# Optimization experiments

Hardware: AMD Instinct MI355X
Metric: run time of the kernel (lower is better)

## Reference

```python
import jax, jax.numpy as jnp
import numpy as np

D_IN, D, H, NL, DFF = 128, 256, 4, 4, 1024
N, B, L = 32768, 64, 672


def setup_inputs() -> dict:
    key = jax.random.key(0)
    ks = jax.random.split(key, 12)
    s = 0.02
    return {
        "dom_embeddings": jax.random.normal(ks[0], (N, D_IN), jnp.float32),
        "dom_to_event_idx": jax.random.randint(ks[1], (N,), 0, B, jnp.int32),
        "batch_size": B,
        "seq_len": L,
        "proj_w": jax.random.normal(ks[2], (D_IN, D), jnp.float32) * s,
        "proj_b": jnp.zeros((D,), jnp.float32),
        "cls_token": jax.random.normal(ks[3], (D,), jnp.float32),
        "ln1_g": jnp.ones((NL, D), jnp.float32),
        "ln1_b": jnp.zeros((NL, D), jnp.float32),
        "qkv_w": jax.random.normal(ks[4], (NL, D, 3 * D), jnp.float32) * s,
        "qkv_b": jnp.zeros((NL, 3 * D), jnp.float32),
        "out_w": jax.random.normal(ks[5], (NL, D, D), jnp.float32) * s,
        "out_b": jnp.zeros((NL, D), jnp.float32),
        "ln2_g": jnp.ones((NL, D), jnp.float32),
        "ln2_b": jnp.zeros((NL, D), jnp.float32),
        "ff1_w": jax.random.normal(ks[6], (NL, D, DFF), jnp.float32) * s,
        "ff1_b": jnp.zeros((NL, DFF), jnp.float32),
        "ff2_w": jax.random.normal(ks[7], (NL, DFF, D), jnp.float32) * s,
        "ff2_b": jnp.zeros((NL, D), jnp.float32),
        "head1_w": jax.random.normal(ks[8], (D, D), jnp.float32) * s,
        "head1_b": jnp.zeros((D,), jnp.float32),
        "head2_w": jax.random.normal(ks[9], (D, 3), jnp.float32) * s,
        "head2_b": jnp.zeros((3,), jnp.float32),
    }


def _ln(x, g, b):
    m = jnp.mean(x, axis=-1, keepdims=True)
    v = jnp.var(x, axis=-1, keepdims=True)
    return (x - m) / jnp.sqrt(v + 1e-5) * g + b


def _forward(dom_embeddings, proj_w, proj_b, cls_token, ln1_g, ln1_b, qkv_w, qkv_b,
             out_w, out_b, ln2_g, ln2_b, ff1_w, ff1_b, ff2_w, ff2_b,
             head1_w, head1_b, head2_w, head2_b, idx, batch_size, seq_len):
    n = idx.shape[0]
    d = proj_w.shape[1]
    dh = d // H
    x = dom_embeddings @ proj_w + proj_b  # (N, d)

    # per-segment rank (replaces the python for-loop): stable argsort + cumsum of counts
    counts = jnp.zeros((batch_size,), jnp.int32).at[idx].add(1)
    starts = jnp.cumsum(counts) - counts
    order = jnp.argsort(idx)  # jax sort is stable -> preserves in-event order
    rank_sorted = jnp.arange(n, dtype=jnp.int32) - starts[idx[order]]
    positions = jnp.zeros((n,), jnp.int32).at[order].set(rank_sorted)

    # scatter into padded batch; slot 0 is cls (note: cls KEY stays masked, as in torch code)
    bt = jnp.zeros((batch_size, seq_len, d), x.dtype).at[:, 0, :].set(cls_token)
    bt = bt.at[idx, positions + 1].set(x)
    pad = jnp.ones((batch_size, seq_len), bool).at[idx, positions + 1].set(False)
    bias = jnp.where(pad, -jnp.inf, 0.0).astype(x.dtype)[:, None, None, :]  # (B,1,1,L)

    h = bt
    for i in range(NL):  # norm_first pre-LN encoder layers
        y = _ln(h, ln1_g[i], ln1_b[i])
        qkv = y @ qkv_w[i] + qkv_b[i]
        q, k, v = jnp.split(qkv, 3, axis=-1)
        q = q.reshape(batch_size, seq_len, H, dh)
        k = k.reshape(batch_size, seq_len, H, dh)
        v = v.reshape(batch_size, seq_len, H, dh)
        scores = jnp.einsum('bqhd,bkhd->bhqk', q, k) * (1.0 / np.sqrt(dh))
        attn = jax.nn.softmax(scores + bias, axis=-1)
        o = jnp.einsum('bhqk,bkhd->bqhd', attn, v).reshape(batch_size, seq_len, d)
        h = h + o @ out_w[i] + out_b[i]
        z = _ln(h, ln2_g[i], ln2_b[i])
        h = h + jax.nn.relu(z @ ff1_w[i] + ff1_b[i]) @ ff2_w[i] + ff2_b[i]

    cls = h[:, 0, :]
    p = jax.nn.relu(cls @ head1_w + head1_b) @ head2_w + head2_b
    return p / jnp.sqrt(jnp.sum(p * p, axis=1, keepdims=True))


def reference(dom_embeddings, dom_to_event_idx, batch_size, seq_len, proj_w, proj_b,
              cls_token, ln1_g, ln1_b, qkv_w, qkv_b, out_w, out_b, ln2_g, ln2_b,
              ff1_w, ff1_b, ff2_w, ff2_b, head1_w, head1_b, head2_w, head2_b):
    return _forward(dom_embeddings, proj_w, proj_b, cls_token, ln1_g, ln1_b, qkv_w,
                    qkv_b, out_w, out_b, ln2_g, ln2_b, ff1_w, ff1_b, ff2_w, ff2_b,
                    head1_w, head1_b, head2_w, head2_b,
                    dom_to_event_idx, batch_size, seq_len)
```

## Files before the change

kernel.cpp:

```cpp
#include <hip/hip_runtime.h>
#include <cstdint>
#include <cstddef>

#define NDOM   32768
#define DIN    128
#define DMODEL 256
#define NHEAD  4
#define NLAYER 4
#define DFFN   1024
#define BATCH  64
#define SEQ    672
#define DHEAD  64
#define MROWS  (BATCH*SEQ)

typedef unsigned short u16;
typedef __attribute__((ext_vector_type(8))) short bf8;
typedef __attribute__((ext_vector_type(4))) float f4;

__device__ inline u16 f2b(float x) {
    union { float f; unsigned u; } c; c.f = x;
    unsigned r = c.u + 0x7fffu + ((c.u >> 16) & 1u);
    return (u16)(r >> 16);
}

__device__ inline void gload16(const void* g, const void* l) {
    __builtin_amdgcn_global_load_lds(
        (const __attribute__((address_space(1))) void*)g,
        (__attribute__((address_space(3))) void*)l, 16, 0, 0);
}


__global__ void k_zero_counts(int* __restrict__ counts) {
    if (threadIdx.x < BATCH) counts[threadIdx.x] = 0;
}

__global__ void k_pos(const int* __restrict__ idx, int* __restrict__ counts,
                      int* __restrict__ pos) {
    int i = blockIdx.x * blockDim.x + threadIdx.x;
    if (i < NDOM) pos[i] = atomicAdd(&counts[idx[i]], 1);
}

__global__ void k_init_h(float* __restrict__ h, const float* __restrict__ cls) {
    const float4* cls4 = (const float4*)cls;
    float4* h4 = (float4*)h;
    const int total4 = MROWS * DMODEL / 4;
    for (int f = blockIdx.x * blockDim.x + threadIdx.x; f < total4;
         f += gridDim.x * blockDim.x) {
        int d4 = f & 63;
        int t  = (f >> 6) % SEQ;
        h4[f] = (t == 0) ? cls4[d4] : make_float4(0.f, 0.f, 0.f, 0.f);
    }
}

__global__ void k_b16(const float* __restrict__ x, u16* __restrict__ y, int n4) {
    int i = blockIdx.x * 256 + threadIdx.x;
    if (i < n4) {
        float4 v = ((const float4*)x)[i];
        ushort4 o;
        o.x = f2b(v.x); o.y = f2b(v.y); o.z = f2b(v.z); o.w = f2b(v.w);
        ((ushort4*)y)[i] = o;
    }
}

__global__ __launch_bounds__(256) void k_wt_all(
    const float* __restrict__ projw, const float* __restrict__ qkvw,
    const float* __restrict__ outw,  const float* __restrict__ ff1w,
    const float* __restrict__ ff2w,
    u16* __restrict__ wpj, u16* __restrict__ wq, u16* __restrict__ wo,
    u16* __restrict__ w1,  u16* __restrict__ w2)
{
    __shared__ float t[64][65];
    const int tile = blockIdx.x;
    const float* W; u16* D; int K, N, local;
    if (tile < 8)        { W = projw; D = wpj; K = 128;  N = 256;  local = tile; }
    else if (tile < 200) { int l = (tile-8)/48;   local = (tile-8)%48;
                           W = qkvw + (size_t)l*196608; D = wq + (size_t)l*196608; K = 256;  N = 768; }
    else if (tile < 264) { int l = (tile-200)/16; local = (tile-200)%16;
                           W = outw + (size_t)l*65536;  D = wo + (size_t)l*65536;  K = 256;  N = 256; }
    else if (tile < 520) { int l = (tile-264)/64; local = (tile-264)%64;
                           W = ff1w + (size_t)l*262144; D = w1 + (size_t)l*262144; K = 256;  N = 1024; }
    else                 { int l = (tile-520)/64; local = (tile-520)%64;
                           W = ff2w + (size_t)l*262144; D = w2 + (size_t)l*262144; K = 1024; N = 256; }
    const int ntn = N >> 6;
    const int tk = local / ntn, tn = local % ntn;
    const int r = threadIdx.x >> 6, c = threadIdx.x & 63;
    #pragma unroll 4
    for (int rr = r; rr < 64; rr += 4)
        t[rr][c] = W[(size_t)(tk*64 + rr) * N + tn*64 + c];
    __syncthreads();
    #pragma unroll 4
    for (int rr = r; rr < 64; rr += 4)
        D[(size_t)(tn*64 + rr) * K + tk*64 + c] = f2b(t[c][rr]);
}

__global__ __launch_bounds__(256) void k_scatter(
    const float* __restrict__ xp, const int* __restrict__ idx,
    const int* __restrict__ pos, float* __restrict__ h)
{
    const int i = blockIdx.x * 4 + (threadIdx.x >> 6);
    const int lane = threadIdx.x & 63;
    const int p = pos[i] + 1;
    if (p >= SEQ) return;
    const size_t row = (size_t)idx[i] * SEQ + p;
    ((float4*)(h + row * DMODEL))[lane] = ((const float4*)(xp + (size_t)i * DMODEL))[lane];
}


__global__ __launch_bounds__(256) void k_ln_bf(
    const float* __restrict__ x, const float* __restrict__ g,
    const float* __restrict__ bt, u16* __restrict__ y)
{
    const int row  = blockIdx.x * 4 + (threadIdx.x >> 6);
    const int lane = threadIdx.x & 63;
    float4 v = ((const float4*)(x + (size_t)row * DMODEL))[lane];
    float s = v.x + v.y + v.z + v.w;
    #pragma unroll
    for (int off = 32; off >= 1; off >>= 1) s += __shfl_xor(s, off);
    const float m = s * (1.f / DMODEL);
    const float d0 = v.x - m, d1 = v.y - m, d2 = v.z - m, d3 = v.w - m;
    float q = d0*d0 + d1*d1 + d2*d2 + d3*d3;
    #pragma unroll
    for (int off = 32; off >= 1; off >>= 1) q += __shfl_xor(q, off);
    const float rstd = rsqrtf(q * (1.f / DMODEL) + 1e-5f);
    const float4 gv = ((const float4*)g)[lane];
    const float4 bv = ((const float4*)bt)[lane];
    ushort4 o;
    o.x = f2b(d0 * rstd * gv.x + bv.x);
    o.y = f2b(d1 * rstd * gv.y + bv.y);
    o.z = f2b(d2 * rstd * gv.z + bv.z);
    o.w = f2b(d3 * rstd * gv.w + bv.w);
    ((ushort4*)(y + (size_t)row * DMODEL))[lane] = o;
}


template<int RELU, int RESID, int OBF, int OF32>
__global__ __launch_bounds__(256) void k_gemm_bf(
    const u16* __restrict__ A, const u16* __restrict__ Bt,
    const float* __restrict__ bias, float* __restrict__ Cf,
    u16* __restrict__ Cb, int K, int N)
{
    __shared__ u16 As[8192];
    __shared__ u16 Bs[8192];
    const int tid = threadIdx.x;
    const int w = tid >> 6, lane = tid & 63;
    const int lr = lane & 15, lg = lane >> 4;
    const int m0 = blockIdx.y * 128, n0 = blockIdx.x * 128;
    const int wm = (w >> 1) * 64, wn = (w & 1) * 64;

    const f4 zf = {0.f, 0.f, 0.f, 0.f};
    f4 acc[4][4];
    #pragma unroll
    for (int i = 0; i < 4; ++i)
        #pragma unroll
        for (int j = 0; j < 4; ++j) acc[i][j] = zf;

    const int srow8 = lane >> 3;
    const int sq = lane & 7;

    for (int k0 = 0; k0 < K; k0 += 64) {
        #pragma unroll
        for (int c = 0; c < 4; ++c) {
            const int chunk = w * 4 + c;
            const int row = chunk * 8 + srow8;
            const int ks = k0 + ((sq ^ (row & 7)) << 3);
            gload16(A  + (size_t)(m0 + row) * K + ks, (const char*)As + chunk * 1024);
            gload16(Bt + (size_t)(n0 + row) * K + ks, (const char*)Bs + chunk * 1024);
        }
        __syncthreads();
        #pragma unroll
        for (int kk = 0; kk < 2; ++kk) {
            bf8 af[4], bg[4];
            #pragma unroll
            for (int f = 0; f < 4; ++f) {
                const int ra = wm + f * 16 + lr;
                af[f] = *(const bf8*)((const char*)As + ra * 128 +
                        ((((kk << 2) | lg) ^ (ra & 7)) << 4));
                const int rb = wn + f * 16 + lr;
                bg[f] = *(const bf8*)((const char*)Bs + rb * 128 +
                        ((((kk << 2) | lg) ^ (rb & 7)) << 4));
            }
            #pragma unroll
            for (int fm = 0; fm < 4; ++fm)
                #pragma unroll
                for (int fn = 0; fn < 4; ++fn)
                    acc[fm][fn] = __builtin_amdgcn_mfma_f32_16x16x32_bf16(
                        af[fm], bg[fn], acc[fm][fn], 0, 0, 0);
        }
        __syncthreads();
    }

    float bv[4];
    #pragma unroll
    for (int fn = 0; fn < 4; ++fn) bv[fn] = bias[n0 + wn + fn * 16 + lr];
    #pragma unroll
    for (int fm = 0; fm < 4; ++fm)
        #pragma unroll
        for (int j = 0; j < 4; ++j) {
            const int row = m0 + wm + fm * 16 + lg * 4 + j;
            #pragma unroll
            for (int fn = 0; fn < 4; ++fn) {
                float v = acc[fm][fn][j] + bv[fn];
                if (RELU) v = fmaxf(v, 0.f);
                const size_t off = (size_t)row * N + n0 + wn + fn * 16 + lr;
                if (RESID) Cf[off] += v;
                if (OF32)  Cf[off] = v;
                if (OBF)   Cb[off] = f2b(v);
            }
        }
}


template<int LNF>
__global__ __launch_bounds__(512) void k_gemm_ln(
    const u16* __restrict__ A, const u16* __restrict__ Bt,
    const float* __restrict__ bias, float* __restrict__ h,
    u16* __restrict__ ybf, const float* __restrict__ lng,
    const float* __restrict__ lnb, int K)
{
    __shared__ u16 As[8192];
    __shared__ u16 Bs[16384];
    __shared__ float red[8][136];
    const int tid = threadIdx.x;
    const int w = tid >> 6, lane = tid & 63;
    const int lr = lane & 15, lg = lane >> 4;
    const int m0 = blockIdx.x * 128;
    const int wm = (w >> 2) * 64, wn = (w & 3) * 64;

    const f4 zf = {0.f, 0.f, 0.f, 0.f};
    f4 acc[4][4];
    #pragma unroll
    for (int i = 0; i < 4; ++i)
        #pragma unroll
        for (int j = 0; j < 4; ++j) acc[i][j] = zf;

    const int srow8 = lane >> 3;
    const int sq = lane & 7;

    for (int k0 = 0; k0 < K; k0 += 64) {
        #pragma unroll
        for (int c = 0; c < 2; ++c) {
            const int chunk = w * 2 + c;
            const int row = chunk * 8 + srow8;
            const int ks = k0 + ((sq ^ (row & 7)) << 3);
            gload16(A + (size_t)(m0 + row) * K + ks, (const char*)As + chunk * 1024);
        }
        #pragma unroll
        for (int c = 0; c < 4; ++c) {
            const int chunk = w * 4 + c;
            const int row = chunk * 8 + srow8;
            const int ks = k0 + ((sq ^ (row & 7)) << 3);
            gload16(Bt + (size_t)row * K + ks, (const char*)Bs + chunk * 1024);
        }
        __syncthreads();
        #pragma unroll
        for (int kk = 0; kk < 2; ++kk) {
            bf8 af[4], bg[4];
            #pragma unroll
            for (int f = 0; f < 4; ++f) {
                const int ra = wm + f * 16 + lr;
                af[f] = *(const bf8*)((const char*)As + ra * 128 +
                        ((((kk << 2) | lg) ^ (ra & 7)) << 4));
                const int rb = wn + f * 16 + lr;
                bg[f] = *(const bf8*)((const char*)Bs + rb * 128 +
                        ((((kk << 2) | lg) ^ (rb & 7)) << 4));
            }
            #pragma unroll
            for (int fm = 0; fm < 4; ++fm)
                #pragma unroll
                for (int fn = 0; fn < 4; ++fn)
                    acc[fm][fn] = __builtin_amdgcn_mfma_f32_16x16x32_bf16(
                        af[fm], bg[fn], acc[fm][fn], 0, 0, 0);
        }
        __syncthreads();
    }

    float bv[4];
    #pragma unroll
    for (int fn = 0; fn < 4; ++fn) bv[fn] = bias[wn + fn * 16 + lr];
    float sr[4][4], s2r[4][4];
    #pragma unroll
    for (int fm = 0; fm < 4; ++fm)
        #pragma unroll
        for (int j = 0; j < 4; ++j) {
            const int row = m0 + wm + fm * 16 + lg * 4 + j;
            float s = 0.f, s2 = 0.f;
            #pragma unroll
            for (int fn = 0; fn < 4; ++fn) {
                float v = acc[fm][fn][j] + bv[fn];
                v += h[(size_t)row * DMODEL + wn + fn * 16 + lr];
                acc[fm][fn][j] = v;
                s += v; s2 += v * v;
            }
            if (LNF) {
                #pragma unroll
                for (int off = 1; off <= 8; off <<= 1) {
                    s  += __shfl_xor(s, off);
                    s2 += __shfl_xor(s2, off);
                }
            }
            sr[fm][j] = s; s2r[fm][j] = s2;
        }

    if (LNF) {
        if (lr == 0) {
            #pragma unroll
            for (int fm = 0; fm < 4; ++fm)
                #pragma unroll
                for (int j = 0; j < 4; ++j) {
                    const int rL = wm + fm * 16 + lg * 4 + j;
                    red[(w & 3) * 2 + 0][rL] = sr[fm][j];
                    red[(w & 3) * 2 + 1][rL] = s2r[fm][j];
                }
        }
        __syncthreads();
        float gl[4], bl[4];
        #pragma unroll
        for (int fn = 0; fn < 4; ++fn) {
            gl[fn] = lng[wn + fn * 16 + lr];
            bl[fn] = lnb[wn + fn * 16 + lr];
        }
        #pragma unroll
        for (int fm = 0; fm < 4; ++fm)
            #pragma unroll
            for (int j = 0; j < 4; ++j) {
                const int rL = wm + fm * 16 + lg * 4 + j;
                const int row = m0 + rL;
                const float S  = red[0][rL] + red[2][rL] + red[4][rL] + red[6][rL];
                const float S2 = red[1][rL] + red[3][rL] + red[5][rL] + red[7][rL];
                const float mean = S * (1.f / DMODEL);
                const float var  = S2 * (1.f / DMODEL) - mean * mean;
                const float rstd = rsqrtf(var + 1e-5f);
                #pragma unroll
                for (int fn = 0; fn < 4; ++fn) {
                    const float v = acc[fm][fn][j];
                    const size_t off = (size_t)row * DMODEL + wn + fn * 16 + lr;
                    h[off] = v;
                    ybf[off] = f2b((v - mean) * rstd * gl[fn] + bl[fn]);
                }
            }
    } else {
        #pragma unroll
        for (int fm = 0; fm < 4; ++fm)
            #pragma unroll
            for (int j = 0; j < 4; ++j) {
                const int row = m0 + wm + fm * 16 + lg * 4 + j;
                #pragma unroll
                for (int fn = 0; fn < 4; ++fn)
                    h[(size_t)row * DMODEL + wn + fn * 16 + lr] = acc[fm][fn][j];
            }
    }
}


__global__ __launch_bounds__(512) void k_attn_mfma(
    const u16* __restrict__ qkv, const int* __restrict__ counts,
    u16* __restrict__ out)
{
    __shared__ u16 Ks[4096];
    __shared__ u16 Vt[4096];
    __shared__ u16 Ps[8][1024];
    const int tid = threadIdx.x;
    const int w = tid >> 6, lane = tid & 63;
    const int lr = lane & 15, lg = lane >> 4;
    const int L = blockIdx.x;
    const int b = (L & 7) * 8 + (L >> 3) / 24;
    const int r = (L >> 3) % 24;
    const int qt = r >> 2, hh = r & 3;
    const int q0 = qt * 128;
    const int kmax = min(counts[b], SEQ - 1);
    if (q0 > kmax) return;
    const int ntiles = (kmax + 64) >> 6;
    const size_t bb = (size_t)b * SEQ;

    const int qrow = q0 + w * 16 + lr;
    const size_t qoff = (bb + (size_t)min(qrow, SEQ - 1)) * 768 + hh * 64 + (lg << 3);
    const bf8 qf0 = *(const bf8*)(qkv + qoff);
    const bf8 qf1 = *(const bf8*)(qkv + qoff + 32);

    const f4 zf = {0.f, 0.f, 0.f, 0.f};
    f4 o_[4];
    #pragma unroll
    for (int fn = 0; fn < 4; ++fn) o_[fn] = zf;
    float mrow = -INFINITY, ssum = 0.f;

    for (int kt = 0; kt < ntiles; ++kt) {
        const int k0 = kt * 64;
        {
            const int row = w * 8 + (lane >> 3);
            const int q = lane & 7;
            const int krow = min(k0 + row, SEQ - 1);
            gload16(qkv + (bb + krow) * 768 + 256 + hh * 64 + ((q ^ (row & 7)) << 3),
                    (const char*)Ks + w * 1024);
        }
        {
            const int kk2 = (tid & 31) * 2;
            const int dh0 = (tid >> 5) * 4;
            const int r0 = min(k0 + kk2, SEQ - 1), r1 = min(k0 + kk2 + 1, SEQ - 1);
            const ushort4 v0 = *(const ushort4*)(qkv + (bb + r0) * 768 + 512 + hh * 64 + dh0);
            const ushort4 v1 = *(const ushort4*)(qkv + (bb + r1) * 768 + 512 + hh * 64 + dh0);
            const u16* pv0 = (const u16*)&v0;
            const u16* pv1 = (const u16*)&v1;
            #pragma unroll
            for (int e = 0; e < 4; ++e) {
                const int d = dh0 + e;
                const unsigned pk = (unsigned)pv0[e] | ((unsigned)pv1[e] << 16);
                *(unsigned*)((char*)Vt + d * 128 +
                    ((((kk2 >> 3) ^ (d & 7)) << 4)) + ((kk2 & 7) << 1)) = pk;
            }
        }
        __syncthreads();

        f4 sf[4];
        #pragma unroll
        for (int fk = 0; fk < 4; ++fk) sf[fk] = zf;
        #pragma unroll
        for (int kk = 0; kk < 2; ++kk) {
            const bf8 qf = kk ? qf1 : qf0;
            #pragma unroll
            for (int fk = 0; fk < 4; ++fk) {
                const int rk = fk * 16 + lr;
                const bf8 kf = *(const bf8*)((const char*)Ks + rk * 128 +
                        ((((kk << 2) | lg) ^ (rk & 7)) << 4));
                sf[fk] = __builtin_amdgcn_mfma_f32_16x16x32_bf16(kf, qf, sf[fk], 0, 0, 0);
            }
        }

        float sv[4][4];
        float pmax = -INFINITY;
        if (k0 >= 1 && k0 + 63 <= kmax) {
            #pragma unroll
            for (int fk = 0; fk < 4; ++fk)
                #pragma unroll
                for (int j = 0; j < 4; ++j) {
                    const float x = sf[fk][j] * 0.125f;
                    sv[fk][j] = x;
                    pmax = fmaxf(pmax, x);
                }
        } else {
            #pragma unroll
            for (int fk = 0; fk < 4; ++fk)
                #pragma unroll
                for (int j = 0; j < 4; ++j) {
                    const int key = k0 + fk * 16 + lg * 4 + j;
                    const float x = (key >= 1 && key <= kmax) ? sf[fk][j] * 0.125f : -INFINITY;
                    sv[fk][j] = x;
                    pmax = fmaxf(pmax, x);
                }
        }
        pmax = fmaxf(pmax, __shfl_xor(pmax, 16));
        pmax = fmaxf(pmax, __shfl_xor(pmax, 32));
        const float mnew = fmaxf(mrow, pmax);
        const float fac = __expf(mrow - mnew);
        mrow = mnew;
        float tsum = 0.f;
        #pragma unroll
        for (int fk = 0; fk < 4; ++fk) {
            const float p0 = __expf(sv[fk][0] - mnew);
            const float p1 = __expf(sv[fk][1] - mnew);
            const float p2 = __expf(sv[fk][2] - mnew);
            const float p3 = __expf(sv[fk][3] - mnew);
            tsum += p0 + p1 + p2 + p3;
            ushort4 pk;
            pk.x = f2b(p0); pk.y = f2b(p1); pk.z = f2b(p2); pk.w = f2b(p3);
            *(ushort4*)((char*)Ps[w] + lr * 128 +
                (((((fk << 1) | (lg >> 1)) ^ (lr & 7)) << 4)) + ((lg & 1) << 3)) = pk;
        }
        tsum += __shfl_xor(tsum, 16);
        tsum += __shfl_xor(tsum, 32);
        ssum = ssum * fac + tsum;

        #pragma unroll
        for (int j = 0; j < 4; ++j) {
            const float fj = __shfl(fac, lg * 4 + j);
            #pragma unroll
            for (int fn = 0; fn < 4; ++fn) o_[fn][j] *= fj;
        }
        __syncthreads();

        #pragma unroll
        for (int kk = 0; kk < 2; ++kk) {
            const bf8 pa = *(const bf8*)((const char*)Ps[w] + lr * 128 +
                    ((((kk << 2) | lg) ^ (lr & 7)) << 4));
            #pragma unroll
            for (int fn = 0; fn < 4; ++fn) {
                const int rv = fn * 16 + lr;
                const bf8 vf = *(const bf8*)((const char*)Vt + rv * 128 +
                        ((((kk << 2) | lg) ^ (rv & 7)) << 4));
                o_[fn] = __builtin_amdgcn_mfma_f32_16x16x32_bf16(pa, vf, o_[fn], 0, 0, 0);
            }
        }
        __syncthreads();
    }

    const float inv = 1.f / ssum;
    #pragma unroll
    for (int j = 0; j < 4; ++j) {
        const float ij = __shfl(inv, lg * 4 + j);
        const int qr = q0 + w * 16 + lg * 4 + j;
        if (qr < SEQ) {
            #pragma unroll
            for (int fn = 0; fn < 4; ++fn)
                out[(bb + qr) * DMODEL + hh * 64 + fn * 16 + lr] = f2b(o_[fn][j] * ij);
        }
    }
}


__global__ __launch_bounds__(256) void k_head(
    const float* __restrict__ h, const float* __restrict__ w1,
    const float* __restrict__ b1, const float* __restrict__ w2,
    const float* __restrict__ b2, float* __restrict__ out)
{
    __shared__ float cbuf[DMODEL];
    __shared__ float p1[DMODEL];
    __shared__ float p2[3];
    const int b = blockIdx.x, tid = threadIdx.x;
    cbuf[tid] = h[(size_t)b * SEQ * DMODEL + tid];
    __syncthreads();
    float acc = b1[tid];
    #pragma unroll 8
    for (int k = 0; k < DMODEL; ++k) acc = fmaf(cbuf[k], w1[k * DMODEL + tid], acc);
    p1[tid] = fmaxf(acc, 0.f);
    __syncthreads();
    if (tid < 3) {
        float a = b2[tid];
        for (int k = 0; k < DMODEL; ++k) a = fmaf(p1[k], w2[k * 3 + tid], a);
        p2[tid] = a;
    }
    __syncthreads();
    if (tid < 3) {
        float n2 = p2[0]*p2[0] + p2[1]*p2[1] + p2[2]*p2[2];
        out[b * 3 + tid] = p2[tid] * rsqrtf(n2);
    }
}


extern "C" void kernel_launch(void* const* d_in, const int* in_sizes, int n_in,
                              void* d_out, int out_size, void* d_ws, size_t ws_size,
                              hipStream_t stream) {
    const float* emb   = (const float*)d_in[0];
    const int*   idx   = (const int*)d_in[1];
    const float* projw = (const float*)d_in[4];
    const float* projb = (const float*)d_in[5];
    const float* cls   = (const float*)d_in[6];
    const float* ln1g  = (const float*)d_in[7];
    const float* ln1b  = (const float*)d_in[8];
    const float* qkvw  = (const float*)d_in[9];
    const float* qkvb  = (const float*)d_in[10];
    const float* outw  = (const float*)d_in[11];
    const float* outb  = (const float*)d_in[12];
    const float* ln2g  = (const float*)d_in[13];
    const float* ln2b  = (const float*)d_in[14];
    const float* ff1w  = (const float*)d_in[15];
    const float* ff1b  = (const float*)d_in[16];
    const float* ff2w  = (const float*)d_in[17];
    const float* ff2b  = (const float*)d_in[18];
    const float* h1w   = (const float*)d_in[19];
    const float* h1b   = (const float*)d_in[20];
    const float* h2w   = (const float*)d_in[21];
    const float* h2b   = (const float*)d_in[22];
    float* out = (float*)d_out;

    char* ws = (char*)d_ws;
    int*   counts = (int*)ws;
    int*   pos    = (int*)(ws + 4096);
    float* h      = (float*)(ws + 135168);
    u16*   ybf    = (u16*)(ws + 44175360);
    u16*   qkvb16 = (u16*)(ws + 66195456);
    u16*   ffb    = (u16*)(ws + 132354048);
    u16*   wq     = (u16*)(ws + 220434432);
    u16*   wo     = (u16*)(ws + 222007296);
    u16*   w1     = (u16*)(ws + 222531584);
    u16*   w2     = (u16*)(ws + 224628736);
    u16*   wpj    = (u16*)(ws + 226725888);
    u16*   embbf  = qkvb16;
    float* xp     = (float*)ffb;

    k_zero_counts<<<1, 64, 0, stream>>>(counts);
    k_pos<<<NDOM / 256, 256, 0, stream>>>(idx, counts, pos);
    k_b16<<<(NDOM * DIN / 4) / 256, 256, 0, stream>>>(emb, embbf, NDOM * DIN / 4);
    k_wt_all<<<776, 256, 0, stream>>>(projw, qkvw, outw, ff1w, ff2w,
                                      wpj, wq, wo, w1, w2);
    k_init_h<<<2688, 256, 0, stream>>>(h, cls);
    k_gemm_bf<0,0,0,1><<<dim3(2, 256), 256, 0, stream>>>(
        embbf, wpj, projb, xp, nullptr, DIN, DMODEL);
    k_scatter<<<NDOM / 4, 256, 0, stream>>>(xp, idx, pos, h);
    k_ln_bf<<<MROWS / 4, 256, 0, stream>>>(h, ln1g, ln1b, ybf);

    for (int l = 0; l < NLAYER; ++l) {
        k_gemm_bf<0,0,1,0><<<dim3(6, 336), 256, 0, stream>>>(
            ybf, wq + (size_t)l * 196608, qkvb + l * 768, nullptr, qkvb16, 256, 768);
        k_attn_mfma<<<1536, 512, 0, stream>>>(qkvb16, counts, ybf);
        k_gemm_ln<1><<<336, 512, 0, stream>>>(
            ybf, wo + (size_t)l * 65536, outb + l * DMODEL, h, ybf,
            ln2g + l * DMODEL, ln2b + l * DMODEL, 256);
        k_gemm_bf<1,0,1,0><<<dim3(8, 336), 256, 0, stream>>>(
            ybf, w1 + (size_t)l * 262144, ff1b + l * DFFN, nullptr, ffb, 256, 1024);
        if (l < NLAYER - 1)
            k_gemm_ln<1><<<336, 512, 0, stream>>>(
                ffb, w2 + (size_t)l * 262144, ff2b + l * DMODEL, h, ybf,
                ln1g + (l + 1) * DMODEL, ln1b + (l + 1) * DMODEL, 1024);
        else
            k_gemm_ln<0><<<336, 512, 0, stream>>>(
                ffb, w2 + (size_t)l * 262144, ff2b + l * DMODEL, h, nullptr,
                nullptr, nullptr, 1024);
    }

    k_head<<<BATCH, 256, 0, stream>>>(h, h1w, h1b, h2w, h2b, out);
}
```

Before: 1.184 ms.

## Pack event rows contiguously to skip padded rows; lazy softmax rescaling

```diff
diff --git a/kernel.cpp b/kernel.cpp
--- a/kernel.cpp
+++ b/kernel.cpp
@@ -11,7 +11,8 @@
 #define BATCH  64
 #define SEQ    672
 #define DHEAD  64
-#define MROWS  (BATCH*SEQ)
+#define MC     33024
+#define MTILES 258
 
 typedef unsigned short u16;
 typedef __attribute__((ext_vector_type(8))) short bf8;
@@ -40,16 +41,31 @@
     if (i < NDOM) pos[i] = atomicAdd(&counts[idx[i]], 1);
 }
 
-__global__ void k_init_h(float* __restrict__ h, const float* __restrict__ cls) {
-    const float4* cls4 = (const float4*)cls;
-    float4* h4 = (float4*)h;
-    const int total4 = MROWS * DMODEL / 4;
-    for (int f = blockIdx.x * blockDim.x + threadIdx.x; f < total4;
-         f += gridDim.x * blockDim.x) {
-        int d4 = f & 63;
-        int t  = (f >> 6) % SEQ;
-        h4[f] = (t == 0) ? cls4[d4] : make_float4(0.f, 0.f, 0.f, 0.f);
-    }
+__global__ void k_base(const int* __restrict__ counts, int* __restrict__ base) {
+    const int lane = threadIdx.x;
+    const int c = counts[lane];
+    int s = c;
+    #pragma unroll
+    for (int off = 1; off < 64; off <<= 1) {
+        int t = __shfl_up(s, off);
+        if (lane >= off) s += t;
+    }
+    base[lane] = lane + (s - c);
+    if (lane == 63) base[64] = 64 + s;
+}
+
+__global__ void k_rmap(const int* __restrict__ idx, const int* __restrict__ pos,
+                       const int* __restrict__ base, int* __restrict__ rmap) {
+    int i = blockIdx.x * 256 + threadIdx.x;
+    if (i < NDOM) {
+        int p = pos[i] + 1;
+        rmap[i] = (p < SEQ) ? base[idx[i]] + p : (MC - 1);
+    }
+}
+
+__global__ void k_init_cls(const int* __restrict__ base, const float* __restrict__ cls,
+                           float* __restrict__ h) {
+    h[(size_t)base[blockIdx.x] * DMODEL + threadIdx.x] = cls[threadIdx.x];
 }
 
 __global__ void k_b16(const float* __restrict__ x, u16* __restrict__ y, int n4) {
@@ -93,18 +109,6 @@
         D[(size_t)(tn*64 + rr) * K + tk*64 + c] = f2b(t[c][rr]);
 }
 
-__global__ __launch_bounds__(256) void k_scatter(
-    const float* __restrict__ xp, const int* __restrict__ idx,
-    const int* __restrict__ pos, float* __restrict__ h)
-{
-    const int i = blockIdx.x * 4 + (threadIdx.x >> 6);
-    const int lane = threadIdx.x & 63;
-    const int p = pos[i] + 1;
-    if (p >= SEQ) return;
-    const size_t row = (size_t)idx[i] * SEQ + p;
-    ((float4*)(h + row * DMODEL))[lane] = ((const float4*)(xp + (size_t)i * DMODEL))[lane];
-}
-
 
 __global__ __launch_bounds__(256) void k_ln_bf(
     const float* __restrict__ x, const float* __restrict__ g,
@@ -133,11 +137,11 @@
 }
 
 
-template<int RELU, int RESID, int OBF, int OF32>
+template<int RELU, int OBF, int OF32, int SCAT>
 __global__ __launch_bounds__(256) void k_gemm_bf(
     const u16* __restrict__ A, const u16* __restrict__ Bt,
     const float* __restrict__ bias, float* __restrict__ Cf,
-    u16* __restrict__ Cb, int K, int N)
+    u16* __restrict__ Cb, const int* __restrict__ rmap, int K, int N)
 {
     __shared__ u16 As[8192];
     __shared__ u16 Bs[8192];
@@ -197,12 +201,12 @@
         #pragma unroll
         for (int j = 0; j < 4; ++j) {
             const int row = m0 + wm + fm * 16 + lg * 4 + j;
+            const int orow = SCAT ? rmap[row] : row;
             #pragma unroll
             for (int fn = 0; fn < 4; ++fn) {
                 float v = acc[fm][fn][j] + bv[fn];
                 if (RELU) v = fmaxf(v, 0.f);
-                const size_t off = (size_t)row * N + n0 + wn + fn * 16 + lr;
-                if (RESID) Cf[off] += v;
+                const size_t off = (size_t)orow * N + n0 + wn + fn * 16 + lr;
                 if (OF32)  Cf[off] = v;
                 if (OBF)   Cb[off] = f2b(v);
             }
@@ -354,7 +358,7 @@
 
 __global__ __launch_bounds__(512) void k_attn_mfma(
     const u16* __restrict__ qkv, const int* __restrict__ counts,
-    u16* __restrict__ out)
+    const int* __restrict__ base, u16* __restrict__ out)
 {
     __shared__ u16 Ks[4096];
     __shared__ u16 Vt[4096];
@@ -370,10 +374,10 @@
     const int kmax = min(counts[b], SEQ - 1);
     if (q0 > kmax) return;
     const int ntiles = (kmax + 64) >> 6;
-    const size_t bb = (size_t)b * SEQ;
+    const size_t bb = (size_t)base[b];
 
     const int qrow = q0 + w * 16 + lr;
-    const size_t qoff = (bb + (size_t)min(qrow, SEQ - 1)) * 768 + hh * 64 + (lg << 3);
+    const size_t qoff = (bb + qrow) * 768 + hh * 64 + (lg << 3);
     const bf8 qf0 = *(const bf8*)(qkv + qoff);
     const bf8 qf1 = *(const bf8*)(qkv + qoff + 32);
 
@@ -388,16 +392,14 @@
         {
             const int row = w * 8 + (lane >> 3);
             const int q = lane & 7;
-            const int krow = min(k0 + row, SEQ - 1);
-            gload16(qkv + (bb + krow) * 768 + 256 + hh * 64 + ((q ^ (row & 7)) << 3),
+            gload16(qkv + (bb + k0 + row) * 768 + 256 + hh * 64 + ((q ^ (row & 7)) << 3),
                     (const char*)Ks + w * 1024);
         }
         {
             const int kk2 = (tid & 31) * 2;
             const int dh0 = (tid >> 5) * 4;
-            const int r0 = min(k0 + kk2, SEQ - 1), r1 = min(k0 + kk2 + 1, SEQ - 1);
-            const ushort4 v0 = *(const ushort4*)(qkv + (bb + r0) * 768 + 512 + hh * 64 + dh0);
-            const ushort4 v1 = *(const ushort4*)(qkv + (bb + r1) * 768 + 512 + hh * 64 + dh0);
+            const ushort4 v0 = *(const ushort4*)(qkv + (bb + k0 + kk2) * 768 + 512 + hh * 64 + dh0);
+            const ushort4 v1 = *(const ushort4*)(qkv + (bb + k0 + kk2 + 1) * 768 + 512 + hh * 64 + dh0);
             const u16* pv0 = (const u16*)&v0;
             const u16* pv1 = (const u16*)&v1;
             #pragma unroll
@@ -449,16 +451,27 @@
         }
         pmax = fmaxf(pmax, __shfl_xor(pmax, 16));
         pmax = fmaxf(pmax, __shfl_xor(pmax, 32));
-        const float mnew = fmaxf(mrow, pmax);
-        const float fac = __expf(mrow - mnew);
-        mrow = mnew;
+
+        if (!__all(pmax <= mrow + 8.f)) {
+            const float mnew = fmaxf(mrow, pmax);
+            const float fac = __expf(mrow - mnew);
+            mrow = mnew;
+            ssum *= fac;
+            #pragma unroll
+            for (int j = 0; j < 4; ++j) {
+                const float fj = __shfl(fac, lg * 4 + j);
+                #pragma unroll
+                for (int fn = 0; fn < 4; ++fn) o_[fn][j] *= fj;
+            }
+        }
+
         float tsum = 0.f;
         #pragma unroll
         for (int fk = 0; fk < 4; ++fk) {
-            const float p0 = __expf(sv[fk][0] - mnew);
-            const float p1 = __expf(sv[fk][1] - mnew);
-            const float p2 = __expf(sv[fk][2] - mnew);
-            const float p3 = __expf(sv[fk][3] - mnew);
+            const float p0 = __expf(sv[fk][0] - mrow);
+            const float p1 = __expf(sv[fk][1] - mrow);
+            const float p2 = __expf(sv[fk][2] - mrow);
+            const float p3 = __expf(sv[fk][3] - mrow);
             tsum += p0 + p1 + p2 + p3;
             ushort4 pk;
             pk.x = f2b(p0); pk.y = f2b(p1); pk.z = f2b(p2); pk.w = f2b(p3);
@@ -467,14 +480,7 @@
         }
         tsum += __shfl_xor(tsum, 16);
         tsum += __shfl_xor(tsum, 32);
-        ssum = ssum * fac + tsum;
-
-        #pragma unroll
-        for (int j = 0; j < 4; ++j) {
-            const float fj = __shfl(fac, lg * 4 + j);
-            #pragma unroll
-            for (int fn = 0; fn < 4; ++fn) o_[fn][j] *= fj;
-        }
+        ssum += tsum;
         __syncthreads();
 
         #pragma unroll
@@ -497,7 +503,7 @@
     for (int j = 0; j < 4; ++j) {
         const float ij = __shfl(inv, lg * 4 + j);
         const int qr = q0 + w * 16 + lg * 4 + j;
-        if (qr < SEQ) {
+        if (qr <= kmax) {
             #pragma unroll
             for (int fn = 0; fn < 4; ++fn)
                 out[(bb + qr) * DMODEL + hh * 64 + fn * 16 + lr] = f2b(o_[fn][j] * ij);
@@ -507,15 +513,16 @@
 
 
 __global__ __launch_bounds__(256) void k_head(
-    const float* __restrict__ h, const float* __restrict__ w1,
-    const float* __restrict__ b1, const float* __restrict__ w2,
-    const float* __restrict__ b2, float* __restrict__ out)
+    const float* __restrict__ h, const int* __restrict__ base,
+    const float* __restrict__ w1, const float* __restrict__ b1,
+    const float* __restrict__ w2, const float* __restrict__ b2,
+    float* __restrict__ out)
 {
     __shared__ float cbuf[DMODEL];
     __shared__ float p1[DMODEL];
     __shared__ float p2[3];
     const int b = blockIdx.x, tid = threadIdx.x;
-    cbuf[tid] = h[(size_t)b * SEQ * DMODEL + tid];
+    cbuf[tid] = h[(size_t)base[b] * DMODEL + tid];
     __syncthreads();
     float acc = b1[tid];
     #pragma unroll 8
@@ -563,48 +570,50 @@
 
     char* ws = (char*)d_ws;
     int*   counts = (int*)ws;
-    int*   pos    = (int*)(ws + 4096);
-    float* h      = (float*)(ws + 135168);
-    u16*   ybf    = (u16*)(ws + 44175360);
-    u16*   qkvb16 = (u16*)(ws + 66195456);
-    u16*   ffb    = (u16*)(ws + 132354048);
-    u16*   wq     = (u16*)(ws + 220434432);
-    u16*   wo     = (u16*)(ws + 222007296);
-    u16*   w1     = (u16*)(ws + 222531584);
-    u16*   w2     = (u16*)(ws + 224628736);
-    u16*   wpj    = (u16*)(ws + 226725888);
-    u16*   embbf  = qkvb16;
-    float* xp     = (float*)ffb;
+    int*   base   = (int*)(ws + 256);
+    int*   pos    = (int*)(ws + 1024);
+    int*   rmap   = (int*)(ws + 132096);
+    float* h      = (float*)(ws + 263168);
+    u16*   ybf    = (u16*)(ws + 34079744);
+    u16*   qkvc   = (u16*)(ws + 50988032);
+    u16*   ffb    = (u16*)(ws + 101712896);
+    u16*   wq     = (u16*)(ws + 169346048);
+    u16*   wo     = (u16*)(ws + 170918912);
+    u16*   w1     = (u16*)(ws + 171443200);
+    u16*   w2     = (u16*)(ws + 173540352);
+    u16*   wpj    = (u16*)(ws + 175637504);
+    u16*   embbf  = qkvc;
 
     k_zero_counts<<<1, 64, 0, stream>>>(counts);
     k_pos<<<NDOM / 256, 256, 0, stream>>>(idx, counts, pos);
+    k_base<<<1, 64, 0, stream>>>(counts, base);
+    k_rmap<<<NDOM / 256, 256, 0, stream>>>(idx, pos, base, rmap);
     k_b16<<<(NDOM * DIN / 4) / 256, 256, 0, stream>>>(emb, embbf, NDOM * DIN / 4);
     k_wt_all<<<776, 256, 0, stream>>>(projw, qkvw, outw, ff1w, ff2w,
                                       wpj, wq, wo, w1, w2);
-    k_init_h<<<2688, 256, 0, stream>>>(h, cls);
-    k_gemm_bf<0,0,0,1><<<dim3(2, 256), 256, 0, stream>>>(
-        embbf, wpj, projb, xp, nullptr, DIN, DMODEL);
-    k_scatter<<<NDOM / 4, 256, 0, stream>>>(xp, idx, pos, h);
-    k_ln_bf<<<MROWS / 4, 256, 0, stream>>>(h, ln1g, ln1b, ybf);
+    k_init_cls<<<BATCH, 256, 0, stream>>>(base, cls, h);
+    k_gemm_bf<0,0,1,1><<<dim3(2, 256), 256, 0, stream>>>(
+        embbf, wpj, projb, h, nullptr, rmap, DIN, DMODEL);
+    k_ln_bf<<<MC / 4, 256, 0, stream>>>(h, ln1g, ln1b, ybf);
 
     for (int l = 0; l < NLAYER; ++l) {
-        k_gemm_bf<0,0,1,0><<<dim3(6, 336), 256, 0, stream>>>(
-            ybf, wq + (size_t)l * 196608, qkvb + l * 768, nullptr, qkvb16, 256, 768);
-        k_attn_mfma<<<1536, 512, 0, stream>>>(qkvb16, counts, ybf);
-        k_gemm_ln<1><<<336, 512, 0, stream>>>(
+        k_gemm_bf<0,1,0,0><<<dim3(6, MTILES), 256, 0, stream>>>(
+            ybf, wq + (size_t)l * 196608, qkvb + l * 768, nullptr, qkvc, nullptr, 256, 768);
+        k_attn_mfma<<<1536, 512, 0, stream>>>(qkvc, counts, base, ybf);
+        k_gemm_ln<1><<<MTILES, 512, 0, stream>>>(
             ybf, wo + (size_t)l * 65536, outb + l * DMODEL, h, ybf,
             ln2g + l * DMODEL, ln2b + l * DMODEL, 256);
-        k_gemm_bf<1,0,1,0><<<dim3(8, 336), 256, 0, stream>>>(
-            ybf, w1 + (size_t)l * 262144, ff1b + l * DFFN, nullptr, ffb, 256, 1024);
+        k_gemm_bf<1,1,0,0><<<dim3(8, MTILES), 256, 0, stream>>>(
+            ybf, w1 + (size_t)l * 262144, ff1b + l * DFFN, nullptr, ffb, nullptr, 256, 1024);
         if (l < NLAYER - 1)
-            k_gemm_ln<1><<<336, 512, 0, stream>>>(
+            k_gemm_ln<1><<<MTILES, 512, 0, stream>>>(
                 ffb, w2 + (size_t)l * 262144, ff2b + l * DMODEL, h, ybf,
                 ln1g + (l + 1) * DMODEL, ln1b + (l + 1) * DMODEL, 1024);
         else
-            k_gemm_ln<0><<<336, 512, 0, stream>>>(
+            k_gemm_ln<0><<<MTILES, 512, 0, stream>>>(
                 ffb, w2 + (size_t)l * 262144, ff2b + l * DMODEL, h, nullptr,
                 nullptr, nullptr, 1024);
     }
 
-    k_head<<<BATCH, 256, 0, stream>>>(h, h1w, h1b, h2w, h2b, out);
-}
+    k_head<<<BATCH, 256, 0, stream>>>(h, base, h1w, h1b, h2w, h2b, out);
+}
```

Result: faster. 1.086 ms (-8.3%).
